# Optimization experiments

Hardware: AMD Instinct MI355X
Metric: run time of the kernel (lower is better)

The kernel has to match this reference:

```python
import jax, jax.numpy as jnp
import numpy as np

D_MODEL = 192
D_STATE = 64
D_CONV = 4
EXPAND = 2
HEADDIM = 64
CHUNK = 256
D_INNER = EXPAND * D_MODEL            # 384
NHEADS = D_INNER // HEADDIM           # 6
CONV_DIM = D_INNER + 2 * D_STATE      # 512 (ngroups=1)
D_IN_PROJ = 2 * D_INNER + 2 * D_STATE + NHEADS  # 902


def setup_inputs() -> dict:
    key = jax.random.key(0)
    ks = jax.random.split(key, 10)
    B, H, W = 8, 64, 64
    rn = lambda k, s, sc: jax.random.normal(k, s, jnp.float32) * sc
    return {
        "x": rn(ks[0], (B, D_MODEL, H, W), 1.0),
        "norm1_w": jnp.ones((D_MODEL,), jnp.float32),
        "norm1_b": jnp.zeros((D_MODEL,), jnp.float32),
        "in_proj_w": rn(ks[1], (D_IN_PROJ, D_MODEL), D_MODEL ** -0.5),
        "conv_w": rn(ks[2], (CONV_DIM, D_CONV), D_CONV ** -0.5),
        "conv_b": jnp.zeros((CONV_DIM,), jnp.float32),
        "dt_bias": jnp.log(jnp.expm1(jax.random.uniform(ks[3], (NHEADS,), jnp.float32, 0.001, 0.1))),
        "A_log": jnp.log(jax.random.uniform(ks[4], (NHEADS,), jnp.float32, 1.0, 16.0)),
        "D_skip": jnp.ones((NHEADS,), jnp.float32),
        "ssm_norm_w": jnp.ones((D_INNER,), jnp.float32),
        "out_proj_w": rn(ks[5], (D_MODEL, D_INNER), D_INNER ** -0.5),
        "norm2_w": jnp.ones((D_MODEL,), jnp.float32),
        "norm2_b": jnp.zeros((D_MODEL,), jnp.float32),
        "ffn_w1": rn(ks[6], (2 * D_MODEL, D_MODEL), D_MODEL ** -0.5),
        "ffn_b1": jnp.zeros((2 * D_MODEL,), jnp.float32),
        "ffn_w2": rn(ks[7], (D_MODEL, 2 * D_MODEL), (2 * D_MODEL) ** -0.5),
        "ffn_b2": jnp.zeros((D_MODEL,), jnp.float32),
    }


def _layernorm(x, w, b, eps=1e-5):
    mu = jnp.mean(x, -1, keepdims=True)
    var = jnp.mean((x - mu) ** 2, -1, keepdims=True)
    return (x - mu) * jax.lax.rsqrt(var + eps) * w + b


def _segsum(a):
    # a: (..., T) -> lower-triangular segment sums, -inf above diagonal
    T = a.shape[-1]
    cs = jnp.cumsum(a, -1)
    d = cs[..., :, None] - cs[..., None, :]
    mask = jnp.tril(jnp.ones((T, T), bool))
    return jnp.where(mask, d, -jnp.inf)


def _ssd(x, A, Bm, Cm):
    # chunked SSD (Mamba2 ssd_minimal). x:(b,l,h,p) pre-scaled by dt; A:(b,l,h)=dt*A_h; Bm,Cm:(b,l,h,n)
    b, l, h, p = x.shape
    c = l // CHUNK
    x = x.reshape(b, c, CHUNK, h, p)
    A = A.reshape(b, c, CHUNK, h).transpose(0, 3, 1, 2)          # (b,h,c,t)
    Bm = Bm.reshape(b, c, CHUNK, h, D_STATE)
    Cm = Cm.reshape(b, c, CHUNK, h, D_STATE)
    A_cs = jnp.cumsum(A, -1)                                      # (b,h,c,t)
    L = jnp.exp(_segsum(A))                                       # (b,h,c,t,t)
    Y_diag = jnp.einsum('bclhn,bcshn,bhcls,bcshp->bclhp', Cm, Bm, L, x)
    decay_states = jnp.exp(A_cs[..., -1:] - A_cs)                 # (b,h,c,t)
    states = jnp.einsum('bclhn,bhcl,bclhp->bchpn', Bm, decay_states, x)
    A_last = jnp.pad(A_cs[..., -1], ((0, 0), (0, 0), (1, 0)))     # (b,h,c+1)
    decay_chunk = jnp.exp(_segsum(A_last))                        # (b,h,c+1,c+1)
    states = jnp.concatenate([jnp.zeros_like(states[:, :1]), states], axis=1)
    new_states = jnp.einsum('bhzc,bchpn->bzhpn', decay_chunk, states)
    states = new_states[:, :-1]                                   # (b,c,h,p,n) inter-chunk init states
    Y_off = jnp.einsum('bclhn,bchpn,bhcl->bclhp', Cm, states, jnp.exp(A_cs))
    return (Y_diag + Y_off).reshape(b, l, h, p)


def _mamba2(u, in_proj_w, conv_w, conv_b, dt_bias, A_log, D_skip, ssm_norm_w, out_proj_w):
    # u: (b, L, d_model) -> (b, L, d_model)
    b, l, _ = u.shape
    zxbcdt = u @ in_proj_w.T                                      # (b,l,902)
    z = zxbcdt[..., :D_INNER]
    xBC = zxbcdt[..., D_INNER:D_INNER + CONV_DIM]
    dt = jax.nn.softplus(zxbcdt[..., -NHEADS:] + dt_bias)         # (b,l,h)
    # causal depthwise conv over sequence
    xBC_t = jax.lax.conv_general_dilated(
        xBC.transpose(0, 2, 1), conv_w[:, None, :], (1,), [(D_CONV - 1, 0)],
        feature_group_count=CONV_DIM, dimension_numbers=('NCH', 'OIH', 'NCH'))
    xBC = jax.nn.silu(xBC_t.transpose(0, 2, 1) + conv_b)
    xs = xBC[..., :D_INNER].reshape(b, l, NHEADS, HEADDIM)
    Bm = jnp.broadcast_to(xBC[..., D_INNER:D_INNER + D_STATE][:, :, None, :], (b, l, NHEADS, D_STATE))
    Cm = jnp.broadcast_to(xBC[..., D_INNER + D_STATE:][:, :, None, :], (b, l, NHEADS, D_STATE))
    A = -jnp.exp(A_log)                                           # (h,)
    y = _ssd(xs * dt[..., None], dt * A, Bm, Cm)
    y = y + xs * D_skip[None, None, :, None]
    y = y.reshape(b, l, D_INNER)
    g = y * jax.nn.silu(z)                                        # gated RMSNorm
    g = g * jax.lax.rsqrt(jnp.mean(g * g, -1, keepdims=True) + 1e-5) * ssm_norm_w
    return g @ out_proj_w.T


def reference(x, norm1_w, norm1_b, in_proj_w, conv_w, conv_b, dt_bias, A_log, D_skip,
              ssm_norm_w, out_proj_w, norm2_w, norm2_b, ffn_w1, ffn_b1, ffn_w2, ffn_b2):
    B, C, H, W = x.shape
    x_flat = x.transpose(0, 2, 3, 1).reshape(B, H * W, C)
    h1 = _layernorm(x_flat, norm1_w, norm1_b)
    # faithful to source: raw reshape (B,HW,C)->(B,C,H,W), then mixer flattens to (B,L,C)
    u = h1.reshape(B, C, H, W).reshape(B, C, H * W).transpose(0, 2, 1)
    m = _mamba2(u, in_proj_w, conv_w, conv_b, dt_bias, A_log, D_skip, ssm_norm_w, out_proj_w)
    m_flat = m.transpose(0, 2, 1).reshape(B, C, H, W).transpose(0, 2, 3, 1).reshape(B, H * W, C)
    x_flat = x_flat + m_flat
    h2 = _layernorm(x_flat, norm2_w, norm2_b)
    f = jax.nn.gelu(h2 @ ffn_w1.T + ffn_b1, approximate=False) @ ffn_w2.T + ffn_b2
    x_flat = x_flat + f
    return x_flat.reshape(B, H, W, C).transpose(0, 3, 1, 2)
```

## Files before the change

kernel.cpp:

```cpp
#include <hip/hip_runtime.h>
#include <hip/hip_bf16.h>

#define BATCH 8
#define CHN   192
#define LEN   4096
#define DI    384
#define NHEAD 6
#define DST   64
#define NCHK  16

typedef __attribute__((ext_vector_type(8))) short short8;
typedef __attribute__((ext_vector_type(4))) short short4v;
typedef __attribute__((ext_vector_type(4))) float f32x4;

__device__ __forceinline__ short f2b(float f) {
  unsigned u = __builtin_bit_cast(unsigned, f);
  unsigned r = (u + 0x7FFFu + ((u >> 16) & 1u)) >> 16;
  return (short)r;
}
__device__ __forceinline__ float bf2f(short s) {
  unsigned u = ((unsigned)(unsigned short)s) << 16;
  return __builtin_bit_cast(float, u);
}

__global__ __launch_bounds__(256) void k_ln1(const float* __restrict__ x,
    const float* __restrict__ w, const float* __restrict__ b, float* __restrict__ h1) {
  __shared__ float s[192][33];
  __shared__ float red[2][32][8];
  __shared__ float mu_s[32], rs_s[32];
  int bb = blockIdx.y;
  int t0 = blockIdx.x * 32;
  int tid = threadIdx.x;
  for (int i = 0; i < 24; ++i) {
    int idx = tid + i * 256;
    int c = idx >> 5, tt = idx & 31;
    s[c][tt] = x[((size_t)bb * CHN + c) * LEN + t0 + tt];
  }
  __syncthreads();
  int tok = tid & 31, part = tid >> 5;
  float sum = 0.f, sq = 0.f;
  for (int c = part * 24; c < part * 24 + 24; ++c) { float v = s[c][tok]; sum += v; sq += v * v; }
  red[0][tok][part] = sum; red[1][tok][part] = sq;
  __syncthreads();
  if (tid < 32) {
    float su = 0.f, qq = 0.f;
    for (int p = 0; p < 8; ++p) { su += red[0][tid][p]; qq += red[1][tid][p]; }
    float mu = su / 192.f;
    float var = qq / 192.f - mu * mu;
    mu_s[tid] = mu; rs_s[tid] = rsqrtf(var + 1e-5f);
  }
  __syncthreads();
  for (int i = 0; i < 24; ++i) {
    int idx = tid + i * 256;
    int c = idx % 192, tt = idx / 192;
    float v = (s[c][tt] - mu_s[tt]) * rs_s[tt] * w[c] + b[c];
    h1[((size_t)bb * LEN + t0 + tt) * CHN + c] = v;
  }
}

__global__ void k_make_u(const float* __restrict__ h1, short* __restrict__ Ub) {
  __shared__ float s[32][33];
  int bb = blockIdx.z;
  int c0 = blockIdx.y * 32;
  int l0 = blockIdx.x * 32;
  int tx = threadIdx.x, ty = threadIdx.y;
  const float* src = h1 + (size_t)bb * (CHN * LEN);
  for (int i = 0; i < 4; ++i)
    s[ty + i * 8][tx] = src[(size_t)(c0 + ty + i * 8) * LEN + l0 + tx];
  __syncthreads();
  short* dstb = Ub + (size_t)bb * (CHN * LEN);
  for (int i = 0; i < 4; ++i)
    dstb[(size_t)(l0 + ty + i * 8) * CHN + c0 + tx] = f2b(s[tx][ty + i * 8]);
}

template <int EPI, int ABF16, int OBF16>
__global__ __launch_bounds__(256) void gemm_mfma(const void* __restrict__ Av,
    const float* __restrict__ W, const float* __restrict__ bias,
    void* __restrict__ Cv, int M, int N, int K, int ldc,
    const float* __restrict__ resid, float* __restrict__ outT) {
  __shared__ short Al[128 * 64];
  __shared__ short Wl[64 * 64];
  int m0 = blockIdx.y * 128, n0 = blockIdx.x * 64;
  int tid = threadIdx.x;
  int lane = tid & 63, wv = tid >> 6;
  int wm = (wv >> 1) * 64, wn = (wv & 1) * 32;
  int l15 = lane & 15, l4 = lane >> 4;
  f32x4 acc[4][2] = {};

  int ra = tid >> 1, ca = (tid & 1) * 32;
  int rw = tid >> 2, cw = (tid & 3) * 16;
  char* ArowL = (char*)Al + ra * 128;
  char* WrowL = (char*)Wl + rw * 128;
  int rxa = (ra & 7) << 4, rxw = (rw & 7) << 4;

  for (int k0 = 0; k0 < K; k0 += 64) {
    if (ABF16) {
      const short* Ag = (const short*)Av + (size_t)(m0 + ra) * K + k0 + ca;
#pragma unroll
      for (int q = 0; q < 4; ++q) {
        short8 pk = *(const short8*)(Ag + q * 8);
        *(short8*)(ArowL + (((ca + q * 8) * 2) ^ rxa)) = pk;
      }
    } else {
      const float* Ag = (const float*)Av + (size_t)(m0 + ra) * K + k0 + ca;
#pragma unroll
      for (int q = 0; q < 4; ++q) {
        float4 v0 = *(const float4*)(Ag + q * 8);
        float4 v1 = *(const float4*)(Ag + q * 8 + 4);
        short8 pk;
        pk[0] = f2b(v0.x); pk[1] = f2b(v0.y); pk[2] = f2b(v0.z); pk[3] = f2b(v0.w);
        pk[4] = f2b(v1.x); pk[5] = f2b(v1.y); pk[6] = f2b(v1.z); pk[7] = f2b(v1.w);
        *(short8*)(ArowL + (((ca + q * 8) * 2) ^ rxa)) = pk;
      }
    }
    {
      const float* Wg = W + (size_t)(n0 + rw) * K + k0 + cw;
#pragma unroll
      for (int q = 0; q < 2; ++q) {
        float4 v0 = *(const float4*)(Wg + q * 8);
        float4 v1 = *(const float4*)(Wg + q * 8 + 4);
        short8 pk;
        pk[0] = f2b(v0.x); pk[1] = f2b(v0.y); pk[2] = f2b(v0.z); pk[3] = f2b(v0.w);
        pk[4] = f2b(v1.x); pk[5] = f2b(v1.y); pk[6] = f2b(v1.z); pk[7] = f2b(v1.w);
        *(short8*)(WrowL + (((cw + q * 8) * 2) ^ rxw)) = pk;
      }
    }
    __syncthreads();
#pragma unroll
    for (int ks = 0; ks < 64; ks += 32) {
      short8 af[4], wf[2];
#pragma unroll
      for (int mf = 0; mf < 4; ++mf) {
        int rr = wm + mf * 16 + l15;
        af[mf] = *(const short8*)((const char*)Al + rr * 128 +
                                  (((ks + l4 * 8) * 2) ^ ((rr & 7) << 4)));
      }
#pragma unroll
      for (int nf = 0; nf < 2; ++nf) {
        int rr = wn + nf * 16 + l15;
        wf[nf] = *(const short8*)((const char*)Wl + rr * 128 +
                                  (((ks + l4 * 8) * 2) ^ ((rr & 7) << 4)));
      }
#pragma unroll
      for (int mf = 0; mf < 4; ++mf)
#pragma unroll
        for (int nf = 0; nf < 2; ++nf)
          acc[mf][nf] = __builtin_amdgcn_mfma_f32_16x16x32_bf16(
              af[mf], wf[nf], acc[mf][nf], 0, 0, 0);
    }
    __syncthreads();
  }
#pragma unroll
  for (int mf = 0; mf < 4; ++mf) {
#pragma unroll
    for (int nf = 0; nf < 2; ++nf) {
      int col = n0 + wn + nf * 16 + l15;
      float bv = (EPI >= 1 && EPI <= 3) ? bias[col] : 0.f;
      if (EPI == 3) {
        int row0 = m0 + wm + mf * 16 + l4 * 4;
        float4 o;
#pragma unroll
        for (int reg = 0; reg < 4; ++reg) {
          int row = row0 + reg;
          ((float*)&o)[reg] = acc[mf][nf][reg] + bv + resid[(size_t)row * CHN + col];
        }
        int bb_l = row0 >> 12, row_l = row0 & 4095;
        *(float4*)&outT[((size_t)bb_l * CHN + col) * LEN + row_l] = o;
      } else if (EPI == 4) {
        int row0 = m0 + wm + mf * 16 + l4 * 4;
        int bb_l = row0 >> 12, row_l = row0 & 4095;
        float4 xv = *(const float4*)&resid[((size_t)bb_l * CHN + col) * LEN + row_l];
#pragma unroll
        for (int reg = 0; reg < 4; ++reg)
          ((float*)Cv)[(size_t)(row0 + reg) * ldc + col] =
              acc[mf][nf][reg] + ((const float*)&xv)[reg];
      } else {
#pragma unroll
        for (int reg = 0; reg < 4; ++reg) {
          int row = m0 + wm + mf * 16 + l4 * 4 + reg;
          float v = acc[mf][nf][reg];
          if (EPI >= 1) v += bv;
          if (EPI == 1) v = 0.5f * v * (1.f + erff(v * 0.70710678118f));
          if (OBF16) ((short*)Cv)[(size_t)row * ldc + col] = f2b(v);
          else       ((float*)Cv)[(size_t)row * ldc + col] = v;
        }
      }
    }
  }
}

__global__ __launch_bounds__(256) void k_dt2(const float* __restrict__ h1,
    const float* __restrict__ win, const float* __restrict__ dt_bias,
    float* __restrict__ dtb) {
  __shared__ float Ut[192][65];
  __shared__ float Wl[6][192];
  int l0 = blockIdx.x * 64, bb = blockIdx.y;
  int tid = threadIdx.x;
  for (int i = tid; i < 6 * 192; i += 256)
    Wl[i / 192][i % 192] = win[(size_t)(896 + i / 192) * 192 + (i % 192)];
  const float* src = h1 + (size_t)bb * (CHN * LEN);
  for (int i = tid; i < 192 * 16; i += 256) {
    int c = i >> 4, q = i & 15;
    float4 v = *(const float4*)&src[(size_t)c * LEN + l0 + q * 4];
    *(float4*)&Ut[c][q * 4] = v;
  }
  __syncthreads();
  int tok = tid & 63, grp = tid >> 6;
  for (int h = grp; h < 6; h += 4) {
    float acc = dt_bias[h];
    for (int c = 0; c < 192; ++c) acc += Ut[c][tok] * Wl[h][c];
    dtb[((size_t)bb * LEN + l0 + tok) * NHEAD + h] =
        (acc > 20.f) ? acc : log1pf(expf(acc));
  }
}

__global__ __launch_bounds__(256) void k_conv(const short* __restrict__ zxs,
    const float* __restrict__ cw, const float* __restrict__ cb,
    short* __restrict__ xbcs) {
  __shared__ float S[67][132];
  int l0 = blockIdx.x * 64, ct = blockIdx.y, bb = blockIdx.z;
  int tid = threadIdx.x;
  int c = (tid & 31) * 4;
  int chb = ct * 128 + c;
  float wr[4][4];
#pragma unroll
  for (int j = 0; j < 4; ++j) {
    float4 w4 = *(const float4*)&cw[(size_t)(chb + j) * 4];
    wr[j][0] = w4.x; wr[j][1] = w4.y; wr[j][2] = w4.z; wr[j][3] = w4.w;
  }
  float4 bc4 = *(const float4*)&cb[chb];
  for (int idx = tid; idx < 67 * 16; idx += 256) {
    int r = idx >> 4, c8 = (idx & 15) * 8;
    int tok = l0 + r - 3;
    if (tok >= 0) {
      short8 v = *(const short8*)&zxs[((size_t)bb * LEN + tok) * 896 + 384 + ct * 128 + c8];
#pragma unroll
      for (int j = 0; j < 8; ++j) S[r][c8 + j] = bf2f(v[j]);
    } else {
#pragma unroll
      for (int j = 0; j < 8; ++j) S[r][c8 + j] = 0.f;
    }
  }
  __syncthreads();
  int t0l = tid >> 5;
#pragma unroll
  for (int it = 0; it < 8; ++it) {
    int tl = it * 8 + t0l;
    float a0 = bc4.x, a1 = bc4.y, a2 = bc4.z, a3 = bc4.w;
#pragma unroll
    for (int k = 0; k < 4; ++k) {
      float4 v = *(const float4*)&S[tl + k][c];
      a0 += v.x * wr[0][k];
      a1 += v.y * wr[1][k];
      a2 += v.z * wr[2][k];
      a3 += v.w * wr[3][k];
    }
    short4v o;
    o[0] = f2b(a0 / (1.f + __expf(-a0)));
    o[1] = f2b(a1 / (1.f + __expf(-a1)));
    o[2] = f2b(a2 / (1.f + __expf(-a2)));
    o[3] = f2b(a3 / (1.f + __expf(-a3)));
    *(short4v*)&xbcs[((size_t)bb * LEN + l0 + tl) * 512 + chb] = o;
  }
}

__global__ __launch_bounds__(256) void k_cumsum(const float* __restrict__ dtb,
    const float* __restrict__ A_log, float* __restrict__ sAg) {
  int cch = blockIdx.x, bb = blockIdx.y;
  int lane = threadIdx.x & 63, wv = threadIdx.x >> 6;
  size_t rowbase = (size_t)bb * LEN + cch * 256;
  for (int h = wv; h < NHEAD; h += 4) {
    float Ah = -expf(A_log[h]);
    float v[4];
#pragma unroll
    for (int i = 0; i < 4; ++i)
      v[i] = dtb[(rowbase + lane * 4 + i) * NHEAD + h] * Ah;
    v[1] += v[0]; v[2] += v[1]; v[3] += v[2];
    float tot = v[3];
    float sc = tot;
    for (int off = 1; off < 64; off <<= 1) {
      float o = __shfl_up(sc, off);
      if (lane >= off) sc += o;
    }
    float excl = sc - tot;
#pragma unroll
    for (int i = 0; i < 4; ++i)
      sAg[(rowbase + lane * 4 + i) * NHEAD + h] = v[i] + excl;
  }
}

__global__ __launch_bounds__(256) void k_xt(const short* __restrict__ xbcs,
    const float* __restrict__ dtb, const float* __restrict__ sAg,
    short* __restrict__ XT, float* __restrict__ states) {
  int cch = blockIdx.x, h = blockIdx.y, bb = blockIdx.z;
  int tid = threadIdx.x;
  int lane = tid & 63, wv = tid >> 6;
  int l15 = lane & 15, l4 = lane >> 4;
  __shared__ float sD[256], sEl[256];
  __shared__ float T[64][68];
  __shared__ short XEl[64 * 64];
  __shared__ short BTl[64 * 64];
  size_t rowbase = (size_t)bb * LEN + cch * 256;
  sD[tid] = dtb[(rowbase + tid) * NHEAD + h];
  {
    float a = sAg[(rowbase + tid) * NHEAD + h];
    float atot = sAg[(rowbase + 255) * NHEAD + h];
    sEl[tid] = __expf(atot - a);
  }
  size_t base_xh = (((size_t)bb * NHEAD + h) * NCHK + cch) * 16384;
  int r = tid >> 2, cq = (tid & 3) * 16;
  int p = tid >> 2, sq = tid & 3;
  int pswz = (p & 7) << 4;
  f32x4 stacc[4] = {};
  for (int ts = 0; ts < 4; ++ts) {
    __syncthreads();
#pragma unroll
    for (int q = 0; q < 2; ++q) {
      short8 v = *(const short8*)&xbcs[(rowbase + ts * 64 + r) * 512 + h * 64 + cq + q * 8];
#pragma unroll
      for (int j = 0; j < 8; ++j) T[r][cq + q * 8 + j] = bf2f(v[j]);
    }
    __syncthreads();
    {
      short8 x0, x1, e0, e1;
#pragma unroll
      for (int j = 0; j < 8; ++j) {
        int sl = sq * 16 + j;
        float f = T[sl][p] * sD[ts * 64 + sl];
        x0[j] = f2b(f);
        e0[j] = f2b(f * sEl[ts * 64 + sl]);
      }
#pragma unroll
      for (int j = 0; j < 8; ++j) {
        int sl = sq * 16 + 8 + j;
        float f = T[sl][p] * sD[ts * 64 + sl];
        x1[j] = f2b(f);
        e1[j] = f2b(f * sEl[ts * 64 + sl]);
      }
      size_t o = base_xh + (size_t)p * 256 + ts * 64 + sq * 16;
      *(short8*)&XT[o] = x0; *(short8*)&XT[o + 8] = x1;
      *(short8*)((char*)XEl + p * 128 + ((sq * 32) ^ pswz)) = e0;
      *(short8*)((char*)XEl + p * 128 + ((sq * 32 + 16) ^ pswz)) = e1;
    }
    __syncthreads();
#pragma unroll
    for (int q = 0; q < 2; ++q) {
      short8 bv = *(const short8*)&xbcs[(rowbase + ts * 64 + r) * 512 + 384 + cq + q * 8];
#pragma unroll
      for (int j = 0; j < 8; ++j) T[r][cq + q * 8 + j] = bf2f(bv[j]);
    }
    __syncthreads();
    {
      short8 b0, b1;
#pragma unroll
      for (int j = 0; j < 8; ++j) b0[j] = f2b(T[sq * 16 + j][p]);
#pragma unroll
      for (int j = 0; j < 8; ++j) b1[j] = f2b(T[sq * 16 + 8 + j][p]);
      *(short8*)((char*)BTl + p * 128 + ((sq * 32) ^ pswz)) = b0;
      *(short8*)((char*)BTl + p * 128 + ((sq * 32 + 16) ^ pswz)) = b1;
    }
    __syncthreads();
#pragma unroll
    for (int ks = 0; ks < 2; ++ks) {
      int rp = wv * 16 + l15;
      short8 aE = *(const short8*)((const char*)XEl + rp * 128 +
                                   (((ks * 32 + l4 * 8) * 2) ^ ((rp & 7) << 4)));
#pragma unroll
      for (int ni = 0; ni < 4; ++ni) {
        int rn = ni * 16 + l15;
        short8 bB = *(const short8*)((const char*)BTl + rn * 128 +
                                     (((ks * 32 + l4 * 8) * 2) ^ ((rn & 7) << 4)));
        stacc[ni] = __builtin_amdgcn_mfma_f32_16x16x32_bf16(aE, bB, stacc[ni], 0, 0, 0);
      }
    }
  }
  size_t stbase = (((size_t)bb * NCHK + cch) * NHEAD + h) * 4096;
#pragma unroll
  for (int ni = 0; ni < 4; ++ni)
#pragma unroll
    for (int reg = 0; reg < 4; ++reg)
      states[stbase + (size_t)(wv * 16 + l4 * 4 + reg) * 64 + ni * 16 + l15] =
          stacc[ni][reg];
}

__global__ void k_scan(const float* __restrict__ states, const float* __restrict__ sAg,
                       short* __restrict__ SinB) {
  int h = blockIdx.x, bb = blockIdx.y;
  int t = threadIdx.x;
  float S[16];
#pragma unroll
  for (int i = 0; i < 16; ++i) S[i] = 0.f;
  for (int z = 0; z < NCHK; ++z) {
    size_t base = (((size_t)bb * NCHK + z) * NHEAD + h) * 4096 + t * 16;
#pragma unroll
    for (int i = 0; i < 16; ++i) SinB[base + i] = f2b(S[i]);
    float az = __expf(sAg[((size_t)bb * LEN + z * 256 + 255) * NHEAD + h]);
#pragma unroll
    for (int i = 0; i < 16; ++i) S[i] = S[i] * az + states[base + i];
  }
}

__global__ __launch_bounds__(256) void k_ssdY(const short* __restrict__ xbcs,
    const short* __restrict__ XT, const short* __restrict__ SinB,
    const float* __restrict__ sAg, short* __restrict__ ybs) {
  int cch = blockIdx.x, h = blockIdx.y, bb = blockIdx.z;
  int tid = threadIdx.x;
  int lane = tid & 63, wv = tid >> 6;
  int l15 = lane & 15, l4 = lane >> 4;
  __shared__ float sA[256];
  __shared__ float sEt[256];
  __shared__ short St[4][64 * 64];
  size_t rowbase = (size_t)bb * LEN + cch * 256;
  {
    float av = sAg[(rowbase + tid) * NHEAD + h];
    sA[tid] = av;
    sEt[tid] = __expf(av);
  }
  __syncthreads();
  size_t base_xh = (((size_t)bb * NHEAD + h) * NCHK + cch) * 16384;
  size_t base_s = (((size_t)bb * NCHK + cch) * NHEAD + h) * 4096;
  int tp = wv;
  short* Sw = St[wv];
  short8 cf[4][2];
#pragma unroll
  for (int ni = 0; ni < 4; ++ni)
#pragma unroll
    for (int ks = 0; ks < 2; ++ks)
      cf[ni][ks] = *(const short8*)&xbcs[(rowbase + tp * 64 + ni * 16 + l15) * 512 +
                                         448 + ks * 32 + l4 * 8];
  float At[4];
#pragma unroll
  for (int ni = 0; ni < 4; ++ni) At[ni] = sA[tp * 64 + ni * 16 + l15];

  f32x4 yacc[4][4];
#pragma unroll
  for (int mi = 0; mi < 4; ++mi) {
    f32x4 yo[4] = {};
#pragma unroll
    for (int ks = 0; ks < 2; ++ks) {
      short8 aS = *(const short8*)&SinB[base_s +
          (size_t)(mi * 16 + l15) * 64 + ks * 32 + l4 * 8];
#pragma unroll
      for (int ni = 0; ni < 4; ++ni)
        yo[ni] = __builtin_amdgcn_mfma_f32_16x16x32_bf16(aS, cf[ni][ks], yo[ni], 0, 0, 0);
    }
#pragma unroll
    for (int ni = 0; ni < 4; ++ni) {
      float et = sEt[tp * 64 + ni * 16 + l15];
#pragma unroll
      for (int reg = 0; reg < 4; ++reg) yacc[mi][ni][reg] = et * yo[ni][reg];
    }
  }
  for (int st = 0; st <= tp; ++st) {
    bool diag = (st == tp);
#pragma unroll
    for (int mi = 0; mi < 4; ++mi) {
      const short* brow = &xbcs[(rowbase + st * 64 + mi * 16 + l15) * 512 + 384 + l4 * 8];
      short8 af0 = *(const short8*)brow;
      short8 af1 = *(const short8*)(brow + 32);
      f32x4 s0[4];
#pragma unroll
      for (int ni = 0; ni < 4; ++ni) {
        f32x4 t = {};
        t = __builtin_amdgcn_mfma_f32_16x16x32_bf16(af0, cf[ni][0], t, 0, 0, 0);
        t = __builtin_amdgcn_mfma_f32_16x16x32_bf16(af1, cf[ni][1], t, 0, 0, 0);
        s0[ni] = t;
      }
      float As[4];
#pragma unroll
      for (int reg = 0; reg < 4; ++reg) As[reg] = sA[st * 64 + mi * 16 + l4 * 4 + reg];
      int s_loc0 = mi * 16 + l4 * 4;
#pragma unroll
      for (int ni = 0; ni < 4; ++ni) {
        int t_loc = ni * 16 + l15;
        short4v pk;
#pragma unroll
        for (int reg = 0; reg < 4; ++reg) {
          float v = __expf(At[ni] - As[reg]) * s0[ni][reg];
          if (diag && (s_loc0 + reg) > t_loc) v = 0.f;
          pk[reg] = f2b(v);
        }
        *(short4v*)((char*)Sw + t_loc * 128 +
                    (((s_loc0 * 2)) ^ ((t_loc & 7) << 4))) = pk;
      }
    }
#pragma unroll
    for (int ks = 0; ks < 2; ++ks) {
      short8 bS[4], aX[4];
#pragma unroll
      for (int ni = 0; ni < 4; ++ni) {
        int rt = ni * 16 + l15;
        bS[ni] = *(const short8*)((const char*)Sw + rt * 128 +
                                  (((ks * 32 + l4 * 8) * 2) ^ ((rt & 7) << 4)));
      }
#pragma unroll
      for (int mi = 0; mi < 4; ++mi)
        aX[mi] = *(const short8*)&XT[base_xh +
            (size_t)(mi * 16 + l15) * 256 + st * 64 + ks * 32 + l4 * 8];
#pragma unroll
      for (int mi = 0; mi < 4; ++mi)
#pragma unroll
        for (int ni = 0; ni < 4; ++ni)
          yacc[mi][ni] = __builtin_amdgcn_mfma_f32_16x16x32_bf16(
              aX[mi], bS[ni], yacc[mi][ni], 0, 0, 0);
    }
  }
#pragma unroll
  for (int ni = 0; ni < 4; ++ni) {
    int tg = tp * 64 + ni * 16 + l15;
#pragma unroll
    for (int mi = 0; mi < 4; ++mi) {
      short4v o;
#pragma unroll
      for (int reg = 0; reg < 4; ++reg) o[reg] = f2b(yacc[mi][ni][reg]);
      *(short4v*)&ybs[(rowbase + tg) * DI + h * 64 + mi * 16 + l4 * 4] = o;
    }
  }
}

__global__ __launch_bounds__(128) void k_gate(const short* __restrict__ ybs,
    const short* __restrict__ zxs, const short* __restrict__ xbcs,
    const float* __restrict__ Dsk, const float* __restrict__ nw,
    short* __restrict__ gn) {
  int row = blockIdx.x;
  int tid = threadIdx.x;
  float g[3]; float sq = 0.f;
#pragma unroll
  for (int i = 0; i < 3; ++i) {
    int d = tid + i * 128;
    int h = d >> 6;
    float z = bf2f(zxs[(size_t)row * 896 + d]);
    float yy = bf2f(ybs[(size_t)row * DI + d]) +
               Dsk[h] * bf2f(xbcs[(size_t)row * 512 + d]);
    float gg = yy * (z / (1.f + expf(-z)));
    g[i] = gg; sq += gg * gg;
  }
  for (int off = 32; off > 0; off >>= 1) sq += __shfl_down(sq, off);
  __shared__ float wsum[2];
  if ((tid & 63) == 0) wsum[tid >> 6] = sq;
  __syncthreads();
  float rs = rsqrtf((wsum[0] + wsum[1]) / 384.f + 1e-5f);
#pragma unroll
  for (int i = 0; i < 3; ++i) {
    int d = tid + i * 128;
    gn[(size_t)row * DI + d] = f2b(g[i] * rs * nw[d]);
  }
}

__global__ __launch_bounds__(64) void k_ln2(const float* __restrict__ r,
    const float* __restrict__ w, const float* __restrict__ b, short* __restrict__ h2) {
  int row = blockIdx.x;
  int tid = threadIdx.x;
  float v[3]; float sum = 0.f;
#pragma unroll
  for (int i = 0; i < 3; ++i) { v[i] = r[(size_t)row * CHN + tid + i * 64]; sum += v[i]; }
  for (int off = 32; off > 0; off >>= 1) sum += __shfl_down(sum, off);
  sum = __shfl(sum, 0);
  float mu = sum / 192.f;
  float sq = 0.f;
#pragma unroll
  for (int i = 0; i < 3; ++i) { float d = v[i] - mu; sq += d * d; }
  for (int off = 32; off > 0; off >>= 1) sq += __shfl_down(sq, off);
  sq = __shfl(sq, 0);
  float rs = rsqrtf(sq / 192.f + 1e-5f);
#pragma unroll
  for (int i = 0; i < 3; ++i) {
    int c = tid + i * 64;
    h2[(size_t)row * CHN + c] = f2b((v[i] - mu) * rs * w[c] + b[c]);
  }
}

extern "C" void kernel_launch(void* const* d_in, const int* in_sizes, int n_in,
                              void* d_out, int out_size, void* d_ws, size_t ws_size,
                              hipStream_t stream) {
  const float* x     = (const float*)d_in[0];
  const float* n1w   = (const float*)d_in[1];
  const float* n1b   = (const float*)d_in[2];
  const float* win   = (const float*)d_in[3];
  const float* cw    = (const float*)d_in[4];
  const float* cb    = (const float*)d_in[5];
  const float* dtbw  = (const float*)d_in[6];
  const float* alog  = (const float*)d_in[7];
  const float* dskip = (const float*)d_in[8];
  const float* snw   = (const float*)d_in[9];
  const float* wout  = (const float*)d_in[10];
  const float* n2w   = (const float*)d_in[11];
  const float* n2b   = (const float*)d_in[12];
  const float* w1    = (const float*)d_in[13];
  const float* b1    = (const float*)d_in[14];
  const float* w2    = (const float*)d_in[15];
  const float* b2    = (const float*)d_in[16];
  float* out = (float*)d_out;

  int g = 8;
  size_t G192, S_ZXH, S_DT, S_XBCH, S_ST;
  for (;;) {
    G192   = (size_t)g * LEN * CHN;
    S_ZXH  = (size_t)g * LEN * 448;
    S_DT   = (size_t)g * LEN * NHEAD;
    S_XBCH = (size_t)g * LEN * 256;
    S_ST   = (size_t)g * NCHK * NHEAD * 4096;
    size_t TOTAL = 2 * G192 + S_ZXH + 2 * S_DT + S_XBCH + G192 / 2 +
                   2 * G192 + S_ST + S_ST / 2 + 64;
    if (TOTAL * 4 <= ws_size) break;
    if (g == 1) return;
    g >>= 1;
  }

  float* ws   = (float*)d_ws;
  float* h1   = ws;
  short* ybs  = (short*)ws;
  short* zxs  = (short*)(ws + 2 * G192);
  float* dtb  = ws + 2 * G192 + S_ZXH;
  float* sag  = dtb + S_DT;
  float* xbp  = sag + S_DT;
  short* xbcs = (short*)xbp;
  short* f1s  = (short*)xbp;
  float* up   = xbp + S_XBCH;
  short* Ubf  = (short*)up;
  short* h2s  = (short*)up;
  float* xtp  = up + G192 / 2;
  short* XT   = (short*)xtp;
  short* gns  = (short*)xtp;
  float* xep  = xtp + G192;
  float* resid= xep;
  float* st   = xep + G192;
  short* SinB = (short*)(st + S_ST);

  const int M = g * LEN;

  for (int b0 = 0; b0 < BATCH; b0 += g) {
    const float* xg  = x   + (size_t)b0 * CHN * LEN;
    float*       og  = out + (size_t)b0 * CHN * LEN;

    k_ln1<<<dim3(LEN / 32, g), 256, 0, stream>>>(xg, n1w, n1b, h1);
    k_make_u<<<dim3(LEN / 32, CHN / 32, g), dim3(32, 8), 0, stream>>>(h1, Ubf);
    gemm_mfma<0, 1, 1><<<dim3(896 / 64, M / 128), 256, 0, stream>>>(
        Ubf, win, nullptr, zxs, M, 896, CHN, 896, nullptr, nullptr);
    k_dt2<<<dim3(LEN / 64, g), 256, 0, stream>>>(h1, win, dtbw, dtb);
    k_conv<<<dim3(LEN / 64, 4, g), 256, 0, stream>>>(zxs, cw, cb, xbcs);
    k_cumsum<<<dim3(NCHK, g), 256, 0, stream>>>(dtb, alog, sag);
    k_xt<<<dim3(NCHK, NHEAD, g), 256, 0, stream>>>(xbcs, dtb, sag, XT, st);
    k_scan<<<dim3(NHEAD, g), 256, 0, stream>>>(st, sag, SinB);
    k_ssdY<<<dim3(NCHK, NHEAD, g), 256, 0, stream>>>(xbcs, XT, SinB, sag, ybs);
    k_gate<<<dim3(M), 128, 0, stream>>>(ybs, zxs, xbcs, dskip, snw, gns);
    gemm_mfma<4, 1, 0><<<dim3(CHN / 64, M / 128), 256, 0, stream>>>(
        gns, wout, nullptr, resid, M, CHN, DI, CHN, xg, nullptr);
    k_ln2<<<dim3(M), 64, 0, stream>>>(resid, n2w, n2b, h2s);
    gemm_mfma<1, 1, 1><<<dim3(DI / 64, M / 128), 256, 0, stream>>>(
        h2s, w1, b1, f1s, M, DI, CHN, DI, nullptr, nullptr);
    gemm_mfma<3, 1, 0><<<dim3(CHN / 64, M / 128), 256, 0, stream>>>(
        f1s, w2, b2, nullptr, M, CHN, DI, CHN, resid, og);
  }
}
```

Measured before the change: 252.0 us.

## Fuse U transpose with dt projection and load-balance ssdY across chunk pairs

Result: no change. 249.3 us (-1.1%).

```diff
diff --git a/kernel.cpp b/kernel.cpp
--- a/kernel.cpp
+++ b/kernel.cpp
@@ -58,19 +58,40 @@
   }
 }
 
-__global__ void k_make_u(const float* __restrict__ h1, short* __restrict__ Ub) {
-  __shared__ float s[32][33];
-  int bb = blockIdx.z;
-  int c0 = blockIdx.y * 32;
-  int l0 = blockIdx.x * 32;
-  int tx = threadIdx.x, ty = threadIdx.y;
+__global__ __launch_bounds__(256) void k_udt(const float* __restrict__ h1,
+    const float* __restrict__ win, const float* __restrict__ dt_bias,
+    short* __restrict__ Ub, float* __restrict__ dtb) {
+  __shared__ float Ut[192][65];
+  __shared__ float Wd[6][192];
+  int l0 = blockIdx.x * 64, bb = blockIdx.y;
+  int tid = threadIdx.x;
+  for (int i = tid; i < 6 * 192; i += 256)
+    Wd[i / 192][i % 192] = win[(size_t)(896 + i / 192) * 192 + (i % 192)];
   const float* src = h1 + (size_t)bb * (CHN * LEN);
-  for (int i = 0; i < 4; ++i)
-    s[ty + i * 8][tx] = src[(size_t)(c0 + ty + i * 8) * LEN + l0 + tx];
+  for (int i = tid; i < 192 * 16; i += 256) {
+    int c = i >> 4, q = i & 15;
+    float4 v = *(const float4*)&src[(size_t)c * LEN + l0 + q * 4];
+    *(float4*)&Ut[c][q * 4] = v;
+  }
   __syncthreads();
-  short* dstb = Ub + (size_t)bb * (CHN * LEN);
-  for (int i = 0; i < 4; ++i)
-    dstb[(size_t)(l0 + ty + i * 8) * CHN + c0 + tx] = f2b(s[tx][ty + i * 8]);
+  {
+    int l = tid >> 2, part = tid & 3;
+    short* dst = Ub + ((size_t)bb * LEN + l0 + l) * CHN + part * 48;
+#pragma unroll
+    for (int q = 0; q < 6; ++q) {
+      short8 pk;
+#pragma unroll
+      for (int j = 0; j < 8; ++j) pk[j] = f2b(Ut[part * 48 + q * 8 + j][l]);
+      *(short8*)&dst[q * 8] = pk;
+    }
+  }
+  int tok = tid & 63, grp = tid >> 6;
+  for (int hh = grp; hh < 6; hh += 4) {
+    float acc = dt_bias[hh];
+    for (int c = 0; c < 192; ++c) acc += Ut[c][tok] * Wd[hh][c];
+    dtb[((size_t)bb * LEN + l0 + tok) * NHEAD + hh] =
+        (acc > 20.f) ? acc : log1pf(expf(acc));
+  }
 }
 
 template <int EPI, int ABF16, int OBF16>
@@ -186,31 +207,6 @@
         }
       }
     }
-  }
-}
-
-__global__ __launch_bounds__(256) void k_dt2(const float* __restrict__ h1,
-    const float* __restrict__ win, const float* __restrict__ dt_bias,
-    float* __restrict__ dtb) {
-  __shared__ float Ut[192][65];
-  __shared__ float Wl[6][192];
-  int l0 = blockIdx.x * 64, bb = blockIdx.y;
-  int tid = threadIdx.x;
-  for (int i = tid; i < 6 * 192; i += 256)
-    Wl[i / 192][i % 192] = win[(size_t)(896 + i / 192) * 192 + (i % 192)];
-  const float* src = h1 + (size_t)bb * (CHN * LEN);
-  for (int i = tid; i < 192 * 16; i += 256) {
-    int c = i >> 4, q = i & 15;
-    float4 v = *(const float4*)&src[(size_t)c * LEN + l0 + q * 4];
-    *(float4*)&Ut[c][q * 4] = v;
-  }
-  __syncthreads();
-  int tok = tid & 63, grp = tid >> 6;
-  for (int h = grp; h < 6; h += 4) {
-    float acc = dt_bias[h];
-    for (int c = 0; c < 192; ++c) acc += Ut[c][tok] * Wl[h][c];
-    dtb[((size_t)bb * LEN + l0 + tok) * NHEAD + h] =
-        (acc > 20.f) ? acc : log1pf(expf(acc));
   }
 }
 
@@ -403,117 +399,126 @@
 __global__ __launch_bounds__(256) void k_ssdY(const short* __restrict__ xbcs,
     const short* __restrict__ XT, const short* __restrict__ SinB,
     const float* __restrict__ sAg, short* __restrict__ ybs) {
-  int cch = blockIdx.x, h = blockIdx.y, bb = blockIdx.z;
+  int cq = blockIdx.x;
+  int h = blockIdx.y, bb = blockIdx.z;
   int tid = threadIdx.x;
   int lane = tid & 63, wv = tid >> 6;
   int l15 = lane & 15, l4 = lane >> 4;
-  __shared__ float sA[256];
-  __shared__ float sEt[256];
+  __shared__ float sA[2][256];
+  __shared__ float sEt[2][256];
   __shared__ short St[4][64 * 64];
-  size_t rowbase = (size_t)bb * LEN + cch * 256;
-  {
-    float av = sAg[(rowbase + tid) * NHEAD + h];
-    sA[tid] = av;
-    sEt[tid] = __expf(av);
+  for (int i = tid; i < 512; i += 256) {
+    int cc = i >> 8, off = i & 255;
+    float av = sAg[((size_t)bb * LEN + (cq * 2 + cc) * 256 + off) * NHEAD + h];
+    sA[cc][off] = av;
+    sEt[cc][off] = __expf(av);
   }
   __syncthreads();
-  size_t base_xh = (((size_t)bb * NHEAD + h) * NCHK + cch) * 16384;
-  size_t base_s = (((size_t)bb * NCHK + cch) * NHEAD + h) * 4096;
-  int tp = wv;
   short* Sw = St[wv];
-  short8 cf[4][2];
-#pragma unroll
-  for (int ni = 0; ni < 4; ++ni)
-#pragma unroll
-    for (int ks = 0; ks < 2; ++ks)
-      cf[ni][ks] = *(const short8*)&xbcs[(rowbase + tp * 64 + ni * 16 + l15) * 512 +
-                                         448 + ks * 32 + l4 * 8];
-  float At[4];
-#pragma unroll
-  for (int ni = 0; ni < 4; ++ni) At[ni] = sA[tp * 64 + ni * 16 + l15];
-
-  f32x4 yacc[4][4];
-#pragma unroll
-  for (int mi = 0; mi < 4; ++mi) {
-    f32x4 yo[4] = {};
-#pragma unroll
-    for (int ks = 0; ks < 2; ++ks) {
-      short8 aS = *(const short8*)&SinB[base_s +
-          (size_t)(mi * 16 + l15) * 64 + ks * 32 + l4 * 8];
-#pragma unroll
-      for (int ni = 0; ni < 4; ++ni)
-        yo[ni] = __builtin_amdgcn_mfma_f32_16x16x32_bf16(aS, cf[ni][ks], yo[ni], 0, 0, 0);
+#pragma unroll
+  for (int j = 0; j < 2; ++j) {
+    int cc = (j == 0) ? (wv & 1) : (1 - (wv & 1));
+    int tp = (j == 0) ? (3 - (wv >> 1)) : (wv >> 1);
+    int cch = cq * 2 + cc;
+    size_t rowbase = (size_t)bb * LEN + cch * 256;
+    size_t base_xh = (((size_t)bb * NHEAD + h) * NCHK + cch) * 16384;
+    size_t base_s = (((size_t)bb * NCHK + cch) * NHEAD + h) * 4096;
+    const float* sAc = sA[cc];
+    const float* sEc = sEt[cc];
+    short8 cf[4][2];
+#pragma unroll
+    for (int ni = 0; ni < 4; ++ni)
+#pragma unroll
+      for (int ks = 0; ks < 2; ++ks)
+        cf[ni][ks] = *(const short8*)&xbcs[(rowbase + tp * 64 + ni * 16 + l15) * 512 +
+                                           448 + ks * 32 + l4 * 8];
+    float At[4];
+#pragma unroll
+    for (int ni = 0; ni < 4; ++ni) At[ni] = sAc[tp * 64 + ni * 16 + l15];
+
+    f32x4 yacc[4][4];
+#pragma unroll
+    for (int mi = 0; mi < 4; ++mi) {
+      f32x4 yo[4] = {};
+#pragma unroll
+      for (int ks = 0; ks < 2; ++ks) {
+        short8 aS = *(const short8*)&SinB[base_s +
+            (size_t)(mi * 16 + l15) * 64 + ks * 32 + l4 * 8];
+#pragma unroll
+        for (int ni = 0; ni < 4; ++ni)
+          yo[ni] = __builtin_amdgcn_mfma_f32_16x16x32_bf16(aS, cf[ni][ks], yo[ni], 0, 0, 0);
+      }
+#pragma unroll
+      for (int ni = 0; ni < 4; ++ni) {
+        float et = sEc[tp * 64 + ni * 16 + l15];
+#pragma unroll
+        for (int reg = 0; reg < 4; ++reg) yacc[mi][ni][reg] = et * yo[ni][reg];
+      }
+    }
+    for (int st = 0; st <= tp; ++st) {
+      bool diag = (st == tp);
+#pragma unroll
+      for (int mi = 0; mi < 4; ++mi) {
+        const short* brow = &xbcs[(rowbase + st * 64 + mi * 16 + l15) * 512 + 384 + l4 * 8];
+        short8 af0 = *(const short8*)brow;
+        short8 af1 = *(const short8*)(brow + 32);
+        f32x4 s0[4];
+#pragma unroll
+        for (int ni = 0; ni < 4; ++ni) {
+          f32x4 t = {};
+          t = __builtin_amdgcn_mfma_f32_16x16x32_bf16(af0, cf[ni][0], t, 0, 0, 0);
+          t = __builtin_amdgcn_mfma_f32_16x16x32_bf16(af1, cf[ni][1], t, 0, 0, 0);
+          s0[ni] = t;
+        }
+        float As[4];
+#pragma unroll
+        for (int reg = 0; reg < 4; ++reg) As[reg] = sAc[st * 64 + mi * 16 + l4 * 4 + reg];
+        int s_loc0 = mi * 16 + l4 * 4;
+#pragma unroll
+        for (int ni = 0; ni < 4; ++ni) {
+          int t_loc = ni * 16 + l15;
+          short4v pk;
+#pragma unroll
+          for (int reg = 0; reg < 4; ++reg) {
+            float v = __expf(At[ni] - As[reg]) * s0[ni][reg];
+            if (diag && (s_loc0 + reg) > t_loc) v = 0.f;
+            pk[reg] = f2b(v);
+          }
+          *(short4v*)((char*)Sw + t_loc * 128 +
+                      (((s_loc0 * 2)) ^ ((t_loc & 7) << 4))) = pk;
+        }
+      }
+#pragma unroll
+      for (int ks = 0; ks < 2; ++ks) {
+        short8 bS[4], aX[4];
+#pragma unroll
+        for (int ni = 0; ni < 4; ++ni) {
+          int rt = ni * 16 + l15;
+          bS[ni] = *(const short8*)((const char*)Sw + rt * 128 +
+                                    (((ks * 32 + l4 * 8) * 2) ^ ((rt & 7) << 4)));
+        }
+#pragma unroll
+        for (int mi = 0; mi < 4; ++mi)
+          aX[mi] = *(const short8*)&XT[base_xh +
+              (size_t)(mi * 16 + l15) * 256 + st * 64 + ks * 32 + l4 * 8];
+#pragma unroll
+        for (int mi = 0; mi < 4; ++mi)
+#pragma unroll
+          for (int ni = 0; ni < 4; ++ni)
+            yacc[mi][ni] = __builtin_amdgcn_mfma_f32_16x16x32_bf16(
+                aX[mi], bS[ni], yacc[mi][ni], 0, 0, 0);
+      }
     }
 #pragma unroll
     for (int ni = 0; ni < 4; ++ni) {
-      float et = sEt[tp * 64 + ni * 16 + l15];
-#pragma unroll
-      for (int reg = 0; reg < 4; ++reg) yacc[mi][ni][reg] = et * yo[ni][reg];
-    }
-  }
-  for (int st = 0; st <= tp; ++st) {
-    bool diag = (st == tp);
-#pragma unroll
-    for (int mi = 0; mi < 4; ++mi) {
-      const short* brow = &xbcs[(rowbase + st * 64 + mi * 16 + l15) * 512 + 384 + l4 * 8];
-      short8 af0 = *(const short8*)brow;
-      short8 af1 = *(const short8*)(brow + 32);
-      f32x4 s0[4];
-#pragma unroll
-      for (int ni = 0; ni < 4; ++ni) {
-        f32x4 t = {};
-        t = __builtin_amdgcn_mfma_f32_16x16x32_bf16(af0, cf[ni][0], t, 0, 0, 0);
-        t = __builtin_amdgcn_mfma_f32_16x16x32_bf16(af1, cf[ni][1], t, 0, 0, 0);
-        s0[ni] = t;
-      }
-      float As[4];
-#pragma unroll
-      for (int reg = 0; reg < 4; ++reg) As[reg] = sA[st * 64 + mi * 16 + l4 * 4 + reg];
-      int s_loc0 = mi * 16 + l4 * 4;
-#pragma unroll
-      for (int ni = 0; ni < 4; ++ni) {
-        int t_loc = ni * 16 + l15;
-        short4v pk;
-#pragma unroll
-        for (int reg = 0; reg < 4; ++reg) {
-          float v = __expf(At[ni] - As[reg]) * s0[ni][reg];
-          if (diag && (s_loc0 + reg) > t_loc) v = 0.f;
-          pk[reg] = f2b(v);
-        }
-        *(short4v*)((char*)Sw + t_loc * 128 +
-                    (((s_loc0 * 2)) ^ ((t_loc & 7) << 4))) = pk;
-      }
-    }
-#pragma unroll
-    for (int ks = 0; ks < 2; ++ks) {
-      short8 bS[4], aX[4];
-#pragma unroll
-      for (int ni = 0; ni < 4; ++ni) {
-        int rt = ni * 16 + l15;
-        bS[ni] = *(const short8*)((const char*)Sw + rt * 128 +
-                                  (((ks * 32 + l4 * 8) * 2) ^ ((rt & 7) << 4)));
-      }
-#pragma unroll
-      for (int mi = 0; mi < 4; ++mi)
-        aX[mi] = *(const short8*)&XT[base_xh +
-            (size_t)(mi * 16 + l15) * 256 + st * 64 + ks * 32 + l4 * 8];
-#pragma unroll
-      for (int mi = 0; mi < 4; ++mi)
-#pragma unroll
-        for (int ni = 0; ni < 4; ++ni)
-          yacc[mi][ni] = __builtin_amdgcn_mfma_f32_16x16x32_bf16(
-              aX[mi], bS[ni], yacc[mi][ni], 0, 0, 0);
-    }
-  }
-#pragma unroll
-  for (int ni = 0; ni < 4; ++ni) {
-    int tg = tp * 64 + ni * 16 + l15;
-#pragma unroll
-    for (int mi = 0; mi < 4; ++mi) {
-      short4v o;
-#pragma unroll
-      for (int reg = 0; reg < 4; ++reg) o[reg] = f2b(yacc[mi][ni][reg]);
-      *(short4v*)&ybs[(rowbase + tg) * DI + h * 64 + mi * 16 + l4 * 4] = o;
+      int tg = tp * 64 + ni * 16 + l15;
+#pragma unroll
+      for (int mi = 0; mi < 4; ++mi) {
+        short4v o;
+#pragma unroll
+        for (int reg = 0; reg < 4; ++reg) o[reg] = f2b(yacc[mi][ni][reg]);
+        *(short4v*)&ybs[(rowbase + tg) * DI + h * 64 + mi * 16 + l4 * 4] = o;
+      }
     }
   }
 }
@@ -634,15 +639,14 @@
     float*       og  = out + (size_t)b0 * CHN * LEN;
 
     k_ln1<<<dim3(LEN / 32, g), 256, 0, stream>>>(xg, n1w, n1b, h1);
-    k_make_u<<<dim3(LEN / 32, CHN / 32, g), dim3(32, 8), 0, stream>>>(h1, Ubf);
+    k_udt<<<dim3(LEN / 64, g), 256, 0, stream>>>(h1, win, dtbw, Ubf, dtb);
     gemm_mfma<0, 1, 1><<<dim3(896 / 64, M / 128), 256, 0, stream>>>(
         Ubf, win, nullptr, zxs, M, 896, CHN, 896, nullptr, nullptr);
-    k_dt2<<<dim3(LEN / 64, g), 256, 0, stream>>>(h1, win, dtbw, dtb);
     k_conv<<<dim3(LEN / 64, 4, g), 256, 0, stream>>>(zxs, cw, cb, xbcs);
     k_cumsum<<<dim3(NCHK, g), 256, 0, stream>>>(dtb, alog, sag);
     k_xt<<<dim3(NCHK, NHEAD, g), 256, 0, stream>>>(xbcs, dtb, sag, XT, st);
     k_scan<<<dim3(NHEAD, g), 256, 0, stream>>>(st, sag, SinB);
-    k_ssdY<<<dim3(NCHK, NHEAD, g), 256, 0, stream>>>(xbcs, XT, SinB, sag, ybs);
+    k_ssdY<<<dim3(NCHK / 2, NHEAD, g), 256, 0, stream>>>(xbcs, XT, SinB, sag, ybs);
     k_gate<<<dim3(M), 128, 0, stream>>>(ybs, zxs, xbcs, dskip, snw, gns);
     gemm_mfma<4, 1, 0><<<dim3(CHN / 64, M / 128), 256, 0, stream>>>(
         gns, wout, nullptr, resid, M, CHN, DI, CHN, xg, nullptr);
```
